# Performance work log

Measured on AMD Instinct MI355X. Metric: run time of the kernel, lower is better.

## Reference

```python
import jax, jax.numpy as jnp
import numpy as np

N = 100000        # nodes
E = 3200000       # edges (avg degree 32)
IN, HID, OUT = 512, 256, 64
K = 10
ALPHA = 0.1


def setup_inputs() -> dict:
    key = jax.random.key(0)
    k1, k2, k3, k4 = jax.random.split(key, 4)
    x = jax.random.normal(k1, (N, IN), dtype=jnp.float32)
    edge_index = jax.random.randint(k2, (2, E), 0, N, dtype=jnp.int64)
    W1 = jax.random.normal(k3, (IN, HID), dtype=jnp.float32) * (1.0 / np.sqrt(IN))
    b1 = jnp.zeros((HID,), dtype=jnp.float32)
    W2 = jax.random.normal(k4, (HID, OUT), dtype=jnp.float32) * (1.0 / np.sqrt(HID))
    b2 = jnp.zeros((OUT,), dtype=jnp.float32)
    return {"x": x, "edge_index": edge_index, "W1": W1, "b1": b1, "W2": W2, "b2": b2}


def reference(x, edge_index, W1, b1, W2, b2):
    # MLP head: Linear -> ReLU -> Linear
    h = jax.nn.relu(x @ W1 + b1)
    h = h @ W2 + b2                                   # [N, OUT]

    # gcn_norm with self-loops: D^-1/2 (A + I) D^-1/2
    src = jnp.concatenate([edge_index[0], jnp.arange(N, dtype=edge_index.dtype)])
    dst = jnp.concatenate([edge_index[1], jnp.arange(N, dtype=edge_index.dtype)])
    deg = jax.ops.segment_sum(jnp.ones_like(src, dtype=h.dtype), dst, num_segments=N)
    dinv = jnp.where(deg > 0, jax.lax.rsqrt(deg), 0.0)
    norm = dinv[src] * dinv[dst]                      # [E+N]

    h0 = h

    def step(h, _):
        msg = h[src] * norm[:, None]                  # gather + edge scale
        agg = jax.ops.segment_sum(msg, dst, num_segments=N)  # scatter-add
        h = (1.0 - ALPHA) * agg + ALPHA * h0          # teleport
        return h, None

    h, _ = jax.lax.scan(step, h, None, length=K)
    return h
```

## Files before the change

kernel.cpp:

```cpp
#include <hip/hip_runtime.h>
#include <hip/hip_bf16.h>
#include <hip/hip_fp16.h>


typedef __bf16 bf16x8 __attribute__((ext_vector_type(8)));
typedef float f32x4 __attribute__((ext_vector_type(4)));

static constexpr int IN = 512, HID = 256, OUT = 64;
static constexpr int LDT = 40;

static __device__ __forceinline__ ushort f2bf(float f) {
  __hip_bfloat16 b = __float2bfloat16(f);
  return *reinterpret_cast<ushort*>(&b);
}
static __device__ __forceinline__ float bf2f(ushort u) {
  unsigned int x = ((unsigned int)u) << 16;
  return __uint_as_float(x);
}
static __device__ __forceinline__ float h15f(unsigned int u) {
  ushort hb = (ushort)(u & 0x7FFFu);
  __half h = *reinterpret_cast<__half*>(&hb);
  return __half2float(h);
}

__global__ void transpose_f32_bf16(const float* __restrict__ in, ushort* __restrict__ out,
                                   int K, int C) {
  int idx = blockIdx.x * 256 + threadIdx.x;
  if (idx < K * C) {
    int n = idx / K, k = idx % K;
    out[idx] = f2bf(in[k * C + n]);
  }
}

__global__ __launch_bounds__(256) void gemm1(const float* __restrict__ X,
                                             const ushort* __restrict__ W1T,
                                             const float* __restrict__ b1,
                                             ushort* __restrict__ h1, int M) {
  __shared__ __align__(16) ushort As[128 * LDT];
  __shared__ __align__(16) ushort Bs[128 * LDT];
  const int tid = threadIdx.x;
  const int m0 = blockIdx.x * 128;
  const int n0 = blockIdx.y * 128;
  const int lane = tid & 63, w = tid >> 6;
  const int wr = w >> 1, wc = w & 1;
  const int lm = lane & 15, lq = lane >> 4;
  const int cB = tid & 3, rB = tid >> 2;
  const int cA = tid & 7, rA = tid >> 3;

  f32x4 acc[4][4] = {};

  for (int k0 = 0; k0 < IN; k0 += 32) {
#pragma unroll
    for (int rr = 0; rr < 4; ++rr) {
      int m = rA + rr * 32;
      int gm = m0 + m; gm = gm < M ? gm : M - 1;
      float4 f = *reinterpret_cast<const float4*>(&X[(size_t)gm * IN + k0 + cA * 4]);
      ushort4 cv;
      cv.x = f2bf(f.x); cv.y = f2bf(f.y); cv.z = f2bf(f.z); cv.w = f2bf(f.w);
      *reinterpret_cast<ushort4*>(&As[m * LDT + cA * 4]) = cv;
    }
#pragma unroll
    for (int rr = 0; rr < 2; ++rr) {
      int n = rB + rr * 64;
      *reinterpret_cast<int4*>(&Bs[n * LDT + cB * 8]) =
          *reinterpret_cast<const int4*>(&W1T[(size_t)(n0 + n) * IN + k0 + cB * 8]);
    }
    __syncthreads();
    bf16x8 af[4], bq[4];
#pragma unroll
    for (int mi = 0; mi < 4; ++mi)
      af[mi] = *reinterpret_cast<const bf16x8*>(&As[(wr * 64 + mi * 16 + lm) * LDT + lq * 8]);
#pragma unroll
    for (int ni = 0; ni < 4; ++ni)
      bq[ni] = *reinterpret_cast<const bf16x8*>(&Bs[(wc * 64 + ni * 16 + lm) * LDT + lq * 8]);
#pragma unroll
    for (int mi = 0; mi < 4; ++mi)
#pragma unroll
      for (int ni = 0; ni < 4; ++ni)
        acc[mi][ni] = __builtin_amdgcn_mfma_f32_16x16x32_bf16(af[mi], bq[ni], acc[mi][ni], 0, 0, 0);
    __syncthreads();
  }

#pragma unroll
  for (int ni = 0; ni < 4; ++ni) {
    int col = n0 + wc * 64 + ni * 16 + lm;
    float bias = b1[col];
#pragma unroll
    for (int mi = 0; mi < 4; ++mi) {
#pragma unroll
      for (int rg = 0; rg < 4; ++rg) {
        int row = m0 + wr * 64 + mi * 16 + lq * 4 + rg;
        if (row < M) {
          float v = acc[mi][ni][rg] + bias;
          v = v > 0.f ? v : 0.f;
          h1[(size_t)row * HID + col] = f2bf(v);
        }
      }
    }
  }
}

__global__ __launch_bounds__(256) void gemm2(const ushort* __restrict__ h1,
                                             const ushort* __restrict__ W2T,
                                             const float* __restrict__ b2,
                                             float* __restrict__ H0f,
                                             ushort* __restrict__ H0b, int M) {
  __shared__ __align__(16) ushort As[128 * LDT];
  __shared__ __align__(16) ushort Bs[64 * LDT];
  const int tid = threadIdx.x;
  const int m0 = blockIdx.x * 128;
  const int lane = tid & 63, w = tid >> 6;
  const int lm = lane & 15, lq = lane >> 4;
  const int c = tid & 3, r = tid >> 2;

  f32x4 acc[2][4] = {};

  for (int k0 = 0; k0 < HID; k0 += 32) {
#pragma unroll
    for (int rr = 0; rr < 2; ++rr) {
      int m = r + rr * 64;
      int gm = m0 + m; gm = gm < M ? gm : M - 1;
      *reinterpret_cast<int4*>(&As[m * LDT + c * 8]) =
          *reinterpret_cast<const int4*>(&h1[(size_t)gm * HID + k0 + c * 8]);
    }
    *reinterpret_cast<int4*>(&Bs[r * LDT + c * 8]) =
        *reinterpret_cast<const int4*>(&W2T[(size_t)r * HID + k0 + c * 8]);
    __syncthreads();
    bf16x8 af[2], bq[4];
#pragma unroll
    for (int mi = 0; mi < 2; ++mi)
      af[mi] = *reinterpret_cast<const bf16x8*>(&As[(w * 32 + mi * 16 + lm) * LDT + lq * 8]);
#pragma unroll
    for (int ni = 0; ni < 4; ++ni)
      bq[ni] = *reinterpret_cast<const bf16x8*>(&Bs[(ni * 16 + lm) * LDT + lq * 8]);
#pragma unroll
    for (int mi = 0; mi < 2; ++mi)
#pragma unroll
      for (int ni = 0; ni < 4; ++ni)
        acc[mi][ni] = __builtin_amdgcn_mfma_f32_16x16x32_bf16(af[mi], bq[ni], acc[mi][ni], 0, 0, 0);
    __syncthreads();
  }

#pragma unroll
  for (int ni = 0; ni < 4; ++ni) {
    int col = ni * 16 + lm;
    float bias = b2[col];
#pragma unroll
    for (int mi = 0; mi < 2; ++mi) {
#pragma unroll
      for (int rg = 0; rg < 4; ++rg) {
        int row = m0 + w * 32 + mi * 16 + lq * 4 + rg;
        if (row < M) {
          float v = acc[mi][ni][rg] + bias;
          H0f[(size_t)row * OUT + col] = v;
          H0b[(size_t)row * OUT + col] = f2bf(v);
        }
      }
    }
  }
}

__global__ void count_deg(const int* __restrict__ ei, int* __restrict__ cnt, int E) {
  int e = blockIdx.x * 256 + threadIdx.x;
  if (e < E) atomicAdd(&cnt[ei[E + e]], 1);
}

__global__ void calc_dinv(const int* __restrict__ cnt, float* __restrict__ dinv, int n) {
  int v = blockIdx.x * 256 + threadIdx.x;
  if (v < n) dinv[v] = rsqrtf((float)cnt[v] + 1.0f);
}

__global__ __launch_bounds__(1024) void scan_kernel(const int* __restrict__ cnt,
                                                    int* __restrict__ offs,
                                                    int* __restrict__ cursor, int n) {
  __shared__ int wsum[16];
  __shared__ int woff[16];
  __shared__ int carry_s;
  const int tid = threadIdx.x;
  const int lane = tid & 63, wid = tid >> 6;
  if (tid == 0) carry_s = 0;
  __syncthreads();
  for (int base = 0; base < n; base += 4096) {
    int i0 = base + tid * 4;
    int x[4];
#pragma unroll
    for (int j = 0; j < 4; ++j) x[j] = (i0 + j < n) ? cnt[i0 + j] : 0;
    int tsum = x[0] + x[1] + x[2] + x[3];
    int val = tsum;
#pragma unroll
    for (int d = 1; d < 64; d <<= 1) {
      int t = __shfl_up(val, d, 64);
      if (lane >= d) val += t;
    }
    if (lane == 63) wsum[wid] = val;
    __syncthreads();
    if (wid == 0) {
      int s = (lane < 16) ? wsum[lane] : 0;
      int sv = s;
#pragma unroll
      for (int d = 1; d < 16; d <<= 1) {
        int t = __shfl_up(sv, d, 64);
        if (lane >= d) sv += t;
      }
      if (lane < 16) woff[lane] = sv - s;
    }
    __syncthreads();
    int excl = carry_s + woff[wid] + (val - tsum);
#pragma unroll
    for (int j = 0; j < 4; ++j) {
      if (i0 + j < n) { offs[i0 + j] = excl; cursor[i0 + j] = excl; }
      excl += x[j];
    }
    __syncthreads();
    if (tid == 1023) carry_s = excl;
    __syncthreads();
  }
  if (tid == 0) offs[n] = carry_s;
}

__global__ void fill_csr(const int* __restrict__ ei, int* __restrict__ cursor,
                         const float* __restrict__ dinv, unsigned int* __restrict__ csr,
                         int E) {
  int e = blockIdx.x * 256 + threadIdx.x;
  if (e < E) {
    int s = ei[e], d = ei[E + e];
    int p = atomicAdd(&cursor[d], 1);
    float w = dinv[s] * dinv[d];
    __half hw = __float2half(w);
    unsigned int hb = *reinterpret_cast<ushort*>(&hw);
    csr[p] = (((unsigned int)s) << 15) | hb;
  }
}

template <bool WRITE_BF>
__global__ __launch_bounds__(256) void prop_step(const float* __restrict__ hinf,
                                                 const ushort* __restrict__ hinb,
                                                 float* __restrict__ houtf,
                                                 ushort* __restrict__ houtb,
                                                 const float* __restrict__ h0,
                                                 const int* __restrict__ offs,
                                                 const unsigned int* __restrict__ csr,
                                                 const float* __restrict__ dinv, int n) {
  int gw = (blockIdx.x * 256 + threadIdx.x) >> 6;
  int lane = threadIdx.x & 63;
  if (gw >= n) return;
  const unsigned int* hin32 = (const unsigned int*)hinb;
  const int c = lane & 31;
  const int half = lane >> 5;
  float alo[8], ahi[8];
#pragma unroll
  for (int k = 0; k < 8; ++k) { alo[k] = 0.f; ahi[k] = 0.f; }
  int e0 = offs[gw], e1 = offs[gw + 1];
  for (int base = e0; base < e1; base += 64) {
    int rem = e1 - base;
    unsigned int my = (lane < rem) ? csr[base + lane] : 0u;
    int cnt = rem < 64 ? rem : 64;
    int cnt32 = (cnt + 31) & ~31;
    for (int j = 0; j < cnt32; j += 32) {
      unsigned int u[16];
#pragma unroll
      for (int k = 0; k < 16; ++k)
        u[k] = (unsigned int)__shfl((int)my, j + 2 * k + half);
      unsigned int v[16];
#pragma unroll
      for (int k = 0; k < 16; ++k)
        v[k] = hin32[(size_t)(u[k] >> 15) * 32 + c];
#pragma unroll
      for (int k = 0; k < 16; ++k) {
        float w = h15f(u[k]);
        float f0 = __uint_as_float(v[k] << 16);
        float f1 = __uint_as_float(v[k] & 0xFFFF0000u);
        alo[k & 7] = fmaf(w, f0, alo[k & 7]);
        ahi[k & 7] = fmaf(w, f1, ahi[k & 7]);
      }
    }
  }
  float a0 = ((alo[0] + alo[1]) + (alo[2] + alo[3])) + ((alo[4] + alo[5]) + (alo[6] + alo[7]));
  float a1 = ((ahi[0] + ahi[1]) + (ahi[2] + ahi[3])) + ((ahi[4] + ahi[5]) + (ahi[6] + ahi[7]));
  a0 += __shfl_xor(a0, 32, 64);
  a1 += __shfl_xor(a1, 32, 64);
  float dv = dinv[gw];
  float2 hf = ((const float2*)hinf)[(size_t)gw * 32 + c];
  float2 h0f = ((const float2*)h0)[(size_t)gw * 32 + c];
  float o0 = 0.9f * (a0 + dv * dv * hf.x) + 0.1f * h0f.x;
  float o1 = 0.9f * (a1 + dv * dv * hf.y) + 0.1f * h0f.y;
  if (half == 0) {
    float2 ov; ov.x = o0; ov.y = o1;
    ((float2*)houtf)[(size_t)gw * 32 + c] = ov;
  } else if (WRITE_BF) {
    unsigned int pk = (unsigned int)f2bf(o0) | ((unsigned int)f2bf(o1) << 16);
    ((unsigned int*)houtb)[(size_t)gw * 32 + c] = pk;
  }
}

extern "C" void kernel_launch(void* const* d_in, const int* in_sizes, int n_in,
                              void* d_out, int out_size, void* d_ws, size_t ws_size,
                              hipStream_t stream) {
  const float* X  = (const float*)d_in[0];
  const int*   EI = (const int*)d_in[1];
  const float* W1 = (const float*)d_in[2];
  const float* b1 = (const float*)d_in[3];
  const float* W2 = (const float*)d_in[4];
  const float* b2 = (const float*)d_in[5];
  float* out = (float*)d_out;

  const int N = in_sizes[0] / IN;
  const int E = in_sizes[1] / 2;

  char* ws = (char*)d_ws;
  size_t o = 0;
  auto alloc = [&](size_t b) {
    char* p = ws + o;
    o = (o + b + 255) & ~(size_t)255;
    return p;
  };
  float*  H0f  = (float*)alloc((size_t)N * OUT * 4);
  ushort* H0b  = (ushort*)alloc((size_t)N * OUT * 2);
  float*  hAf  = (float*)alloc((size_t)N * OUT * 4);
  ushort* hAb  = (ushort*)alloc((size_t)N * OUT * 2);
  float*  hBf  = (float*)alloc((size_t)N * OUT * 4);
  ushort* hBb  = (ushort*)alloc((size_t)N * OUT * 2);
  ushort* h1   = (ushort*)alloc((size_t)N * HID * 2);
  ushort* W1T  = (ushort*)alloc((size_t)IN * HID * 2);
  ushort* W2T  = (ushort*)alloc((size_t)HID * OUT * 2);
  int*    cnt  = (int*)alloc((size_t)N * 4);
  int*    offs = (int*)alloc((size_t)(N + 1) * 4);
  int*    curs = (int*)alloc((size_t)N * 4);
  float*  dinv = (float*)alloc((size_t)N * 4);
  unsigned int* csr = (unsigned int*)alloc((size_t)E * 4);
  (void)ws_size; (void)n_in; (void)out_size;

  transpose_f32_bf16<<<(IN * HID + 255) / 256, 256, 0, stream>>>(W1, W1T, IN, HID);
  transpose_f32_bf16<<<(HID * OUT + 255) / 256, 256, 0, stream>>>(W2, W2T, HID, OUT);

  gemm1<<<dim3((N + 127) / 128, HID / 128), 256, 0, stream>>>(X, W1T, b1, h1, N);
  gemm2<<<(N + 127) / 128, 256, 0, stream>>>(h1, W2T, b2, H0f, H0b, N);

  hipMemsetAsync(cnt, 0, (size_t)N * 4, stream);
  count_deg<<<(E + 255) / 256, 256, 0, stream>>>(EI, cnt, E);
  calc_dinv<<<(N + 255) / 256, 256, 0, stream>>>(cnt, dinv, N);
  scan_kernel<<<1, 1024, 0, stream>>>(cnt, offs, curs, N);
  fill_csr<<<(E + 255) / 256, 256, 0, stream>>>(EI, curs, dinv, csr, E);

  const int pgrid = (N * OUT + 255) / 256;
  prop_step<true><<<pgrid, 256, 0, stream>>>(H0f, H0b, hAf, hAb, H0f, offs, csr, dinv, N);
  for (int i = 0; i < 4; ++i) {
    prop_step<true><<<pgrid, 256, 0, stream>>>(hAf, hAb, hBf, hBb, H0f, offs, csr, dinv, N);
    prop_step<true><<<pgrid, 256, 0, stream>>>(hBf, hBb, hAf, hAb, H0f, offs, csr, dinv, N);
  }
  prop_step<false><<<pgrid, 256, 0, stream>>>(hAf, hAb, out, nullptr, H0f, offs, csr, dinv, N);
}
```

Before: 1.368 ms.

## Prefetch next K-tile into registers and double K-step in both MLP GEMMs

Result: slower. 1.413 ms (+3.3%).

```diff
diff --git a/kernel.cpp b/kernel.cpp
--- a/kernel.cpp
+++ b/kernel.cpp
@@ -7,7 +7,7 @@
 typedef float f32x4 __attribute__((ext_vector_type(4)));
 
 static constexpr int IN = 512, HID = 256, OUT = 64;
-static constexpr int LDT = 40;
+static constexpr int LDT = 72;
 
 static __device__ __forceinline__ ushort f2bf(float f) {
   __hip_bfloat16 b = __float2bfloat16(f);
@@ -44,41 +44,70 @@
   const int lane = tid & 63, w = tid >> 6;
   const int wr = w >> 1, wc = w & 1;
   const int lm = lane & 15, lq = lane >> 4;
-  const int cB = tid & 3, rB = tid >> 2;
-  const int cA = tid & 7, rA = tid >> 3;
+  const int cA = tid & 15, rA = tid >> 4;
+  const int cB = tid & 7, rB = tid >> 3;
+
+  float4 pa[8];
+  int4 pb[4];
+
+  auto LOADA = [&](int k0) {
+#pragma unroll
+    for (int rr = 0; rr < 8; ++rr) {
+      int gm = m0 + rA + rr * 16; gm = gm < M ? gm : M - 1;
+      pa[rr] = *reinterpret_cast<const float4*>(&X[(size_t)gm * IN + k0 + cA * 4]);
+    }
+  };
+  auto LOADB = [&](int k0) {
+#pragma unroll
+    for (int rr = 0; rr < 4; ++rr) {
+      int n = rB + rr * 32;
+      pb[rr] = *reinterpret_cast<const int4*>(&W1T[(size_t)(n0 + n) * IN + k0 + cB * 8]);
+    }
+  };
+  auto STORE = [&]() {
+#pragma unroll
+    for (int rr = 0; rr < 8; ++rr) {
+      ushort4 cv;
+      cv.x = f2bf(pa[rr].x); cv.y = f2bf(pa[rr].y);
+      cv.z = f2bf(pa[rr].z); cv.w = f2bf(pa[rr].w);
+      *reinterpret_cast<ushort4*>(&As[(rA + rr * 16) * LDT + cA * 4]) = cv;
+    }
+#pragma unroll
+    for (int rr = 0; rr < 4; ++rr)
+      *reinterpret_cast<int4*>(&Bs[(rB + rr * 32) * LDT + cB * 8]) = pb[rr];
+  };
 
   f32x4 acc[4][4] = {};
 
-  for (int k0 = 0; k0 < IN; k0 += 32) {
-#pragma unroll
-    for (int rr = 0; rr < 4; ++rr) {
-      int m = rA + rr * 32;
-      int gm = m0 + m; gm = gm < M ? gm : M - 1;
-      float4 f = *reinterpret_cast<const float4*>(&X[(size_t)gm * IN + k0 + cA * 4]);
-      ushort4 cv;
-      cv.x = f2bf(f.x); cv.y = f2bf(f.y); cv.z = f2bf(f.z); cv.w = f2bf(f.w);
-      *reinterpret_cast<ushort4*>(&As[m * LDT + cA * 4]) = cv;
-    }
-#pragma unroll
-    for (int rr = 0; rr < 2; ++rr) {
-      int n = rB + rr * 64;
-      *reinterpret_cast<int4*>(&Bs[n * LDT + cB * 8]) =
-          *reinterpret_cast<const int4*>(&W1T[(size_t)(n0 + n) * IN + k0 + cB * 8]);
-    }
-    __syncthreads();
-    bf16x8 af[4], bq[4];
-#pragma unroll
-    for (int mi = 0; mi < 4; ++mi)
-      af[mi] = *reinterpret_cast<const bf16x8*>(&As[(wr * 64 + mi * 16 + lm) * LDT + lq * 8]);
-#pragma unroll
-    for (int ni = 0; ni < 4; ++ni)
-      bq[ni] = *reinterpret_cast<const bf16x8*>(&Bs[(wc * 64 + ni * 16 + lm) * LDT + lq * 8]);
-#pragma unroll
-    for (int mi = 0; mi < 4; ++mi)
+  LOADA(0); LOADB(0);
+  STORE();
+  __syncthreads();
+
+  for (int k0 = 64; k0 <= IN; k0 += 64) {
+    const bool more = (k0 < IN);
+    if (more) { LOADA(k0); LOADB(k0); }
+#pragma unroll
+    for (int kk = 0; kk < 2; ++kk) {
+      bf16x8 af[4], bq[4];
+#pragma unroll
+      for (int mi = 0; mi < 4; ++mi)
+        af[mi] = *reinterpret_cast<const bf16x8*>(
+            &As[(wr * 64 + mi * 16 + lm) * LDT + kk * 32 + lq * 8]);
 #pragma unroll
       for (int ni = 0; ni < 4; ++ni)
-        acc[mi][ni] = __builtin_amdgcn_mfma_f32_16x16x32_bf16(af[mi], bq[ni], acc[mi][ni], 0, 0, 0);
-    __syncthreads();
+        bq[ni] = *reinterpret_cast<const bf16x8*>(
+            &Bs[(wc * 64 + ni * 16 + lm) * LDT + kk * 32 + lq * 8]);
+#pragma unroll
+      for (int mi = 0; mi < 4; ++mi)
+#pragma unroll
+        for (int ni = 0; ni < 4; ++ni)
+          acc[mi][ni] = __builtin_amdgcn_mfma_f32_16x16x32_bf16(af[mi], bq[ni], acc[mi][ni], 0, 0, 0);
+    }
+    __syncthreads();
+    if (more) {
+      STORE();
+      __syncthreads();
+    }
   }
 
 #pragma unroll
@@ -111,34 +140,63 @@
   const int m0 = blockIdx.x * 128;
   const int lane = tid & 63, w = tid >> 6;
   const int lm = lane & 15, lq = lane >> 4;
-  const int c = tid & 3, r = tid >> 2;
+  const int cA = tid & 7, rA = tid >> 3;
+
+  int4 pa[4];
+  int4 pb[2];
+
+  auto LOADA = [&](int k0) {
+#pragma unroll
+    for (int rr = 0; rr < 4; ++rr) {
+      int gm = m0 + rA + rr * 32; gm = gm < M ? gm : M - 1;
+      pa[rr] = *reinterpret_cast<const int4*>(&h1[(size_t)gm * HID + k0 + cA * 8]);
+    }
+  };
+  auto LOADB = [&](int k0) {
+#pragma unroll
+    for (int rr = 0; rr < 2; ++rr)
+      pb[rr] = *reinterpret_cast<const int4*>(&W2T[(size_t)(rA + rr * 32) * HID + k0 + cA * 8]);
+  };
+  auto STORE = [&]() {
+#pragma unroll
+    for (int rr = 0; rr < 4; ++rr)
+      *reinterpret_cast<int4*>(&As[(rA + rr * 32) * LDT + cA * 8]) = pa[rr];
+#pragma unroll
+    for (int rr = 0; rr < 2; ++rr)
+      *reinterpret_cast<int4*>(&Bs[(rA + rr * 32) * LDT + cA * 8]) = pb[rr];
+  };
 
   f32x4 acc[2][4] = {};
 
-  for (int k0 = 0; k0 < HID; k0 += 32) {
-#pragma unroll
-    for (int rr = 0; rr < 2; ++rr) {
-      int m = r + rr * 64;
-      int gm = m0 + m; gm = gm < M ? gm : M - 1;
-      *reinterpret_cast<int4*>(&As[m * LDT + c * 8]) =
-          *reinterpret_cast<const int4*>(&h1[(size_t)gm * HID + k0 + c * 8]);
-    }
-    *reinterpret_cast<int4*>(&Bs[r * LDT + c * 8]) =
-        *reinterpret_cast<const int4*>(&W2T[(size_t)r * HID + k0 + c * 8]);
-    __syncthreads();
-    bf16x8 af[2], bq[4];
-#pragma unroll
-    for (int mi = 0; mi < 2; ++mi)
-      af[mi] = *reinterpret_cast<const bf16x8*>(&As[(w * 32 + mi * 16 + lm) * LDT + lq * 8]);
-#pragma unroll
-    for (int ni = 0; ni < 4; ++ni)
-      bq[ni] = *reinterpret_cast<const bf16x8*>(&Bs[(ni * 16 + lm) * LDT + lq * 8]);
-#pragma unroll
-    for (int mi = 0; mi < 2; ++mi)
+  LOADA(0); LOADB(0);
+  STORE();
+  __syncthreads();
+
+  for (int k0 = 64; k0 <= HID; k0 += 64) {
+    const bool more = (k0 < HID);
+    if (more) { LOADA(k0); LOADB(k0); }
+#pragma unroll
+    for (int kk = 0; kk < 2; ++kk) {
+      bf16x8 af[2], bq[4];
+#pragma unroll
+      for (int mi = 0; mi < 2; ++mi)
+        af[mi] = *reinterpret_cast<const bf16x8*>(
+            &As[(w * 32 + mi * 16 + lm) * LDT + kk * 32 + lq * 8]);
 #pragma unroll
       for (int ni = 0; ni < 4; ++ni)
-        acc[mi][ni] = __builtin_amdgcn_mfma_f32_16x16x32_bf16(af[mi], bq[ni], acc[mi][ni], 0, 0, 0);
-    __syncthreads();
+        bq[ni] = *reinterpret_cast<const bf16x8*>(
+            &Bs[(ni * 16 + lm) * LDT + kk * 32 + lq * 8]);
+#pragma unroll
+      for (int mi = 0; mi < 2; ++mi)
+#pragma unroll
+        for (int ni = 0; ni < 4; ++ni)
+          acc[mi][ni] = __builtin_amdgcn_mfma_f32_16x16x32_bf16(af[mi], bq[ni], acc[mi][ni], 0, 0, 0);
+    }
+    __syncthreads();
+    if (more) {
+      STORE();
+      __syncthreads();
+    }
   }
 
 #pragma unroll
```
